# Kernel tuning notes

Measured on AMD Instinct MI355X. Metric: run time of the kernel, lower is better.

Reference implementation:

```python
import jax, jax.numpy as jnp
import numpy as np

N, M, D = 8192, 8192, 512

def setup_inputs() -> dict:
    key = jax.random.key(0)
    ks = jax.random.split(key, 8)
    s = 1.0 / np.sqrt(D)
    return {
        "x": jax.random.normal(ks[0], (N, D), jnp.float32),
        "domain_x": jax.random.normal(ks[1], (M, D), jnp.float32),
        "Wq": jax.random.normal(ks[2], (D, D), jnp.float32) * s,
        "bq": jax.random.normal(ks[3], (D,), jnp.float32) * s,
        "Wk": jax.random.normal(ks[4], (D, D), jnp.float32) * s,
        "bk": jax.random.normal(ks[5], (D,), jnp.float32) * s,
        "Wv": jax.random.normal(ks[6], (D, D), jnp.float32) * s,
        "bv": jax.random.normal(ks[7], (D,), jnp.float32) * s,
    }

def reference(x, domain_x, Wq, bq, Wk, bk, Wv, bv):
    # torch Linear: y = x @ W^T + b
    q = x @ Wq.T + bq            # [N, D]
    k = domain_x @ Wk.T + bk     # [M, D]
    v = domain_x @ Wv.T + bv     # [M, D]
    scale = jnp.sqrt(jnp.asarray(k.shape[-1], q.dtype))
    scores = q @ k.T             # [N, M]
    attn = jax.nn.softmax(scores / scale, axis=-1)
    return attn @ v              # [N, D]
```

## Files before the change

kernel.cpp:

```cpp
#include <hip/hip_runtime.h>
#include <stdint.h>


#define DEV __device__ __forceinline__

typedef short short8 __attribute__((ext_vector_type(8)));
typedef float floatx4 __attribute__((ext_vector_type(4)));
typedef unsigned int uintx4 __attribute__((ext_vector_type(4)));
typedef unsigned short ushortx4 __attribute__((ext_vector_type(4)));

constexpr int NN = 8192;
constexpr int MM = 8192;
constexpr int DD = 512;
constexpr float SCALE2 = 0.0637587160f;
constexpr float DEFER_THR = 6.0f;

#define NEG_INF (-__builtin_inff())

#if defined(__has_builtin)
#if __has_builtin(__builtin_amdgcn_exp2f)
#define EXP2F(x) __builtin_amdgcn_exp2f(x)
#else
#define EXP2F(x) exp2f(x)
#endif
#else
#define EXP2F(x) exp2f(x)
#endif

DEV unsigned short f2bf(float f) {
  unsigned u = __builtin_bit_cast(unsigned, f);
  return (unsigned short)((u + 0x7FFFu + ((u >> 16) & 1u)) >> 16);
}
DEV float bf2f(unsigned short h) {
  unsigned u = ((unsigned)h) << 16;
  return __builtin_bit_cast(float, u);
}

DEV short8 ld_s8(const void* p) {
  short8 v; __builtin_memcpy(&v, __builtin_assume_aligned(p, 16), 16); return v;
}
DEV uintx4 ld_u4(const void* p) {
  uintx4 v; __builtin_memcpy(&v, __builtin_assume_aligned(p, 16), 16); return v;
}
DEV void st_u4(void* p, uintx4 v) {
  __builtin_memcpy(__builtin_assume_aligned(p, 16), &v, 16);
}
DEV void st_us4(void* p, ushortx4 v) {
  __builtin_memcpy(__builtin_assume_aligned(p, 8), &v, 8);
}
DEV float4 ld_f4(const void* p) {
  float4 v; __builtin_memcpy(&v, __builtin_assume_aligned(p, 16), 16); return v;
}

DEV void async_lds16(const void* g, const void* l) {
  __builtin_amdgcn_global_load_lds(
      (const __attribute__((address_space(1))) unsigned int*)g,
      (__attribute__((address_space(3))) unsigned int*)l, 16, 0, 0);
}

__global__ void prep_w(const float* __restrict__ Wq, const float* __restrict__ Wk,
                       const float* __restrict__ Wv, unsigned short* __restrict__ Wb) {
  const int z = blockIdx.z;
  const float* src = (z == 0) ? Wq : (z == 1) ? Wk : Wv;
  unsigned short* dst = Wb + (size_t)z * DD * DD;
  size_t idx = ((size_t)blockIdx.x * 256 + threadIdx.x) * 8;
  float4 a = ld_f4(src + idx);
  float4 b = ld_f4(src + idx + 4);
  ushortx4 lo = {f2bf(a.x), f2bf(a.y), f2bf(a.z), f2bf(a.w)};
  ushortx4 hi = {f2bf(b.x), f2bf(b.y), f2bf(b.z), f2bf(b.w)};
  st_us4(dst + idx, lo);
  st_us4(dst + idx + 4, hi);
}

__global__ __launch_bounds__(256, 2)
void qkv_proj(const float* __restrict__ x, const float* __restrict__ dx,
              const unsigned short* __restrict__ Wb,
              const float* __restrict__ bq, const float* __restrict__ bk,
              const float* __restrict__ bv,
              unsigned short* __restrict__ Qb, unsigned short* __restrict__ Kb,
              unsigned short* __restrict__ VTb) {
  const int z = blockIdx.z;
  const float* A = (z == 0) ? x : dx;
  const unsigned short* W = Wb + (size_t)z * DD * DD;
  const float* bias = (z == 0) ? bq : (z == 1) ? bk : bv;

  const int r0 = blockIdx.x * 64;
  const int c0 = blockIdx.y * 256;
  const int tid = threadIdx.x;
  const int lane = tid & 63;
  const int wave = tid >> 6;
  const int lr = lane & 15;
  const int quad = lane >> 4;

  __shared__ __align__(16) unsigned short As[64 * 64];
  __shared__ __align__(16) unsigned short Ws[256 * 64];

  floatx4 o[16];
#pragma unroll
  for (int i = 0; i < 16; ++i) o[i] = {0.f, 0.f, 0.f, 0.f};

  for (int k0 = 0; k0 < DD; k0 += 64) {
#pragma unroll
    for (int i = 0; i < 4; ++i) {
      int idx = i * 256 + tid;
      int r = idx >> 4, c4 = idx & 15;
      float4 v = ld_f4(A + (size_t)(r0 + r) * DD + k0 + c4 * 4);
      ushortx4 pk = {f2bf(v.x), f2bf(v.y), f2bf(v.z), f2bf(v.w)};
      st_us4(&As[r * 64 + (((c4 >> 1) ^ (r & 7)) * 8) + (c4 & 1) * 4], pk);
    }
#pragma unroll
    for (int i = 0; i < 8; ++i) {
      int idx = i * 256 + tid;
      int r = idx >> 3, c = idx & 7;
      uintx4 v = ld_u4(W + (size_t)(c0 + r) * DD + k0 + c * 8);
      st_u4(&Ws[r * 64 + ((c ^ (r & 7)) * 8)], v);
    }
    __syncthreads();

    short8 a[2];
#pragma unroll
    for (int ks = 0; ks < 2; ++ks)
      a[ks] = ld_s8(&As[(wave * 16 + lr) * 64 + (((ks * 4 + quad) ^ (lr & 7)) * 8)]);
#pragma unroll
    for (int ct = 0; ct < 16; ++ct) {
#pragma unroll
      for (int ks = 0; ks < 2; ++ks) {
        short8 b = ld_s8(&Ws[(ct * 16 + lr) * 64 + (((ks * 4 + quad) ^ (lr & 7)) * 8)]);
        o[ct] = __builtin_amdgcn_mfma_f32_16x16x32_bf16(a[ks], b, o[ct], 0, 0, 0);
      }
    }
    __syncthreads();
  }

#pragma unroll
  for (int ct = 0; ct < 16; ++ct) {
    int col = c0 + ct * 16 + lr;
    float bv_ = bias[col];
    int rowb = r0 + wave * 16 + quad * 4;
    if (z == 2) {
      ushortx4 pk = {f2bf(o[ct][0] + bv_), f2bf(o[ct][1] + bv_),
                     f2bf(o[ct][2] + bv_), f2bf(o[ct][3] + bv_)};
      st_us4(VTb + (size_t)col * MM + rowb, pk);
    } else {
      unsigned short* Outp = (z == 0) ? Qb : Kb;
      float sc = (z == 0) ? SCALE2 : 1.f;
#pragma unroll
      for (int r = 0; r < 4; ++r)
        Outp[(size_t)(rowb + r) * DD + col] = f2bf((o[ct][r] + bv_) * sc);
    }
  }
}

template <int SPLITS_, int LOG2S_>
__global__ __launch_bounds__(256, 2)
void flash_attn(const unsigned short* __restrict__ Qb,
                const unsigned short* __restrict__ Kb,
                const unsigned short* __restrict__ VTb,
                unsigned short* __restrict__ Opart,
                float* __restrict__ Mpart, float* __restrict__ Lpart) {
  constexpr int MT = MM / SPLITS_;
  constexpr int ITERS = MT / 64;
  const int lin = blockIdx.x;
  const int split = lin & (SPLITS_ - 1);
  const int n0 = (lin >> LOG2S_) * 64;
  const int m_begin = split * MT;

  const int tid = threadIdx.x;
  const int lane = tid & 63;
  const int wave = tid >> 6;
  const int lr = lane & 15;
  const int quad = lane >> 4;

  __shared__ __align__(16) unsigned short sKV[33280];
  __shared__ __align__(16) unsigned short sP[64 * 76];
  __shared__ float sAlpha[64];
  __shared__ int sNeed;

  if (tid == 0) sNeed = 0;

  short8 qf[16];
  {
    const unsigned short* qptr = Qb + (size_t)(n0 + wave * 16 + lr) * DD + quad * 8;
#pragma unroll
    for (int ks = 0; ks < 16; ++ks) qf[ks] = ld_s8(qptr + ks * 32);
  }

  const int vrb = lane >> 3;
  const int vcb = ((lane & 7) ^ vrb) * 8;
  const unsigned short* vsrc0 = VTb + (size_t)(wave * 128 + vrb) * MM + vcb;
  unsigned short* vdst0 = &sKV[wave * 16 * 512];

  floatx4 o[32];
#pragma unroll
  for (int i = 0; i < 32; ++i) o[i] = {0.f, 0.f, 0.f, 0.f};
  float mrow[4] = {NEG_INF, NEG_INF, NEG_INF, NEG_INF};
  float lrow[4] = {0.f, 0.f, 0.f, 0.f};

  for (int it = 0; it < ITERS; ++it) {
    const int m0 = m_begin + it * 64;

#pragma unroll
    for (int i = 0; i < 16; ++i) {
      const int r = wave * 16 + i;
      async_lds16(Kb + (size_t)(m0 + r) * DD + lane * 8, &sKV[r * 520]);
    }
    __syncthreads();

    floatx4 s[4];
#pragma unroll
    for (int ct = 0; ct < 4; ++ct) s[ct] = {0.f, 0.f, 0.f, 0.f};
    __builtin_amdgcn_s_setprio(1);
#pragma unroll
    for (int ks = 0; ks < 16; ++ks) {
      const unsigned short* kb = &sKV[ks * 32 + quad * 8];
#pragma unroll
      for (int ct = 0; ct < 4; ++ct) {
        short8 b = ld_s8(kb + (ct * 16 + lr) * 520);
        s[ct] = __builtin_amdgcn_mfma_f32_16x16x32_bf16(qf[ks], b, s[ct], 0, 0, 0);
      }
    }
    __builtin_amdgcn_s_setprio(0);
    __syncthreads();

    {
      const unsigned short* src = vsrc0 + m0;
#pragma unroll
      for (int j = 0; j < 16; ++j)
        async_lds16(src + (size_t)j * 8 * MM, vdst0 + j * 512);
    }

    float alpha[4];
    bool anyresc = false;
#pragma unroll
    for (int r = 0; r < 4; ++r) {
      float mx = fmaxf(fmaxf(s[0][r], s[1][r]), fmaxf(s[2][r], s[3][r]));
      mx = fmaxf(mx, __shfl_xor(mx, 1));
      mx = fmaxf(mx, __shfl_xor(mx, 2));
      mx = fmaxf(mx, __shfl_xor(mx, 4));
      mx = fmaxf(mx, __shfl_xor(mx, 8));
      float mnew = (mx > mrow[r] + DEFER_THR) ? mx : mrow[r];
      alpha[r] = EXP2F(mrow[r] - mnew);
      anyresc = anyresc || (mnew != mrow[r]);
      mrow[r] = mnew;
      float rs = 0.f;
#pragma unroll
      for (int ct = 0; ct < 4; ++ct) {
        float p = EXP2F(s[ct][r] - mnew);
        s[ct][r] = p;
        rs += p;
      }
      rs += __shfl_xor(rs, 1);
      rs += __shfl_xor(rs, 2);
      rs += __shfl_xor(rs, 4);
      rs += __shfl_xor(rs, 8);
      lrow[r] = lrow[r] * alpha[r] + rs;
    }
    if (__any(anyresc)) {
      if (lane == 0) sNeed = 1;
    }
    if (lr == 0) {
#pragma unroll
      for (int r = 0; r < 4; ++r) sAlpha[wave * 16 + quad * 4 + r] = alpha[r];
    }

#pragma unroll
    for (int ct = 0; ct < 4; ++ct)
#pragma unroll
      for (int r = 0; r < 4; ++r)
        sP[(wave * 16 + quad * 4 + r) * 76 + ct * 16 + lr] = f2bf(s[ct][r]);

    __syncthreads();

    if (sNeed) {
      floatx4 af[4];
#pragma unroll
      for (int rt = 0; rt < 4; ++rt) {
        float4 t = ld_f4(&sAlpha[rt * 16 + quad * 4]);
        af[rt] = {t.x, t.y, t.z, t.w};
      }
#pragma unroll
      for (int rt = 0; rt < 4; ++rt)
#pragma unroll
        for (int ct = 0; ct < 8; ++ct)
#pragma unroll
          for (int r = 0; r < 4; ++r) o[rt * 8 + ct][r] *= af[rt][r];
    }

    __builtin_amdgcn_s_setprio(1);
#pragma unroll
    for (int ks = 0; ks < 2; ++ks) {
      short8 pa[4];
#pragma unroll
      for (int rt = 0; rt < 4; ++rt)
        pa[rt] = ld_s8(&sP[(rt * 16 + lr) * 76 + ks * 32 + quad * 8]);
#pragma unroll
      for (int ct = 0; ct < 8; ++ct) {
        const int r = wave * 128 + ct * 16 + lr;
        short8 b = ld_s8(&sKV[r * 64 + (((ks * 4 + quad) ^ (lr & 7)) * 8)]);
#pragma unroll
        for (int rt = 0; rt < 4; ++rt)
          o[rt * 8 + ct] = __builtin_amdgcn_mfma_f32_16x16x32_bf16(pa[rt], b,
                                                                   o[rt * 8 + ct], 0, 0, 0);
      }
    }
    __builtin_amdgcn_s_setprio(0);
    __syncthreads();
    if (tid == 0) sNeed = 0;
  }

  unsigned short* op = Opart + (size_t)split * NN * DD;
#pragma unroll
  for (int rt = 0; rt < 4; ++rt)
#pragma unroll
    for (int ct = 0; ct < 8; ++ct) {
      int row = n0 + rt * 16 + quad * 4;
      int col = wave * 128 + ct * 16 + lr;
#pragma unroll
      for (int r = 0; r < 4; ++r)
        op[(size_t)(row + r) * DD + col] = f2bf(o[rt * 8 + ct][r]);
    }
  const int grow = n0 + wave * 16 + quad * 4;
  if (lr == 0) {
#pragma unroll
    for (int r = 0; r < 4; ++r) {
      Mpart[split * NN + grow + r] = mrow[r];
      Lpart[split * NN + grow + r] = lrow[r];
    }
  }
}

template <int SPLITS_>
__global__ void combine_kernel(const unsigned short* __restrict__ Op,
                               const float* __restrict__ Mp,
                               const float* __restrict__ Lp,
                               float* __restrict__ out) {
  constexpr size_t NDv = (size_t)NN * DD;
  size_t base = ((size_t)blockIdx.x * 256 + threadIdx.x) * 8;
  int n = (int)(base >> 9);
  float mv[SPLITS_];
  float ms = NEG_INF;
#pragma unroll
  for (int s = 0; s < SPLITS_; ++s) {
    mv[s] = Mp[s * NN + n];
    ms = fmaxf(ms, mv[s]);
  }
  float num[8];
#pragma unroll
  for (int j = 0; j < 8; ++j) num[j] = 0.f;
  float den = 0.f;
#pragma unroll
  for (int s = 0; s < SPLITS_; ++s) {
    float w = EXP2F(mv[s] - ms);
    den += w * Lp[s * NN + n];
    uintx4 u = ld_u4(Op + s * NDv + base);
#pragma unroll
    for (int j = 0; j < 4; ++j) {
      num[2 * j]     += w * bf2f((unsigned short)(u[j] & 0xffffu));
      num[2 * j + 1] += w * bf2f((unsigned short)(u[j] >> 16));
    }
  }
  float inv = 1.f / den;
  float4 o0 = {num[0] * inv, num[1] * inv, num[2] * inv, num[3] * inv};
  float4 o1 = {num[4] * inv, num[5] * inv, num[6] * inv, num[7] * inv};
  __builtin_memcpy(__builtin_assume_aligned(out + base, 16), &o0, 16);
  __builtin_memcpy(__builtin_assume_aligned(out + base + 4, 16), &o1, 16);
}

extern "C" void kernel_launch(void* const* d_in, const int* in_sizes, int n_in,
                              void* d_out, int out_size, void* d_ws, size_t ws_size,
                              hipStream_t stream) {
  const float* x  = (const float*)d_in[0];
  const float* dx = (const float*)d_in[1];
  const float* Wq = (const float*)d_in[2];
  const float* bq = (const float*)d_in[3];
  const float* Wk = (const float*)d_in[4];
  const float* bk = (const float*)d_in[5];
  const float* Wv = (const float*)d_in[6];
  const float* bv = (const float*)d_in[7];
  float* out = (float*)d_out;

  const size_t ND = (size_t)NN * DD;
  const size_t WBE = (size_t)3 * DD * DD;
  unsigned short* Qb  = (unsigned short*)d_ws;
  unsigned short* Kb  = Qb + ND;
  unsigned short* VTb = Kb + ND;
  unsigned short* Wb  = VTb + ND;
  unsigned short* Op  = Wb + WBE;

  auto bytes_for = [&](size_t S) {
    return (3 * ND + WBE + S * ND) * 2 + S * (size_t)NN * 8;
  };
  const int splits = (ws_size >= bytes_for(4)) ? 4 : 2;
  float* Mp = (float*)(Op + (size_t)splits * ND);
  float* Lp = Mp + (size_t)splits * NN;

  hipLaunchKernelGGL(prep_w, dim3(DD * DD / 2048, 1, 3), dim3(256), 0, stream,
                     Wq, Wk, Wv, Wb);
  hipLaunchKernelGGL(qkv_proj, dim3(NN / 64, 2, 3), dim3(256), 0, stream,
                     x, dx, Wb, bq, bk, bv, Qb, Kb, VTb);
  if (splits == 4) {
    hipLaunchKernelGGL((flash_attn<4, 2>), dim3(NN / 64 * 4), dim3(256), 0, stream,
                       Qb, Kb, VTb, Op, Mp, Lp);
    hipLaunchKernelGGL(combine_kernel<4>, dim3((unsigned)(ND / 2048)), dim3(256), 0, stream,
                       Op, Mp, Lp, out);
  } else {
    hipLaunchKernelGGL((flash_attn<2, 1>), dim3(NN / 64 * 2), dim3(256), 0, stream,
                       Qb, Kb, VTb, Op, Mp, Lp);
    hipLaunchKernelGGL(combine_kernel<2>, dim3((unsigned)(ND / 2048)), dim3(256), 0, stream,
                       Op, Mp, Lp, out);
  }
}
```

Before: 337.4 us.

## Load V fragments directly from global in MFMA layout, prefetch next K tile

The V projection is now written in a blocked layout that matches the MFMA B-operand fragment order, so the PV product reads V straight from global memory into registers instead of staging it through LDS. The freed LDS buffer lets the next K tile be prefetched asynchronously during softmax, and the trailing barrier per iteration is removed by double-buffering the rescale flag. The sP row pitch drops from 76 to 72. This trades LDS traffic and barriers for more global/L2 loads on the critical path of the PV MFMAs, and may raise latency exposure or bank conflicts.

Measured after the change: 431.2 us. 27.8% more time.

```diff
diff --git a/kernel.cpp b/kernel.cpp
--- a/kernel.cpp
+++ b/kernel.cpp
@@ -14,6 +14,7 @@
 constexpr int DD = 512;
 constexpr float SCALE2 = 0.0637587160f;
 constexpr float DEFER_THR = 6.0f;
+constexpr int SP = 72;
 
 #define NEG_INF (-__builtin_inff())
 
@@ -140,7 +141,11 @@
     if (z == 2) {
       ushortx4 pk = {f2bf(o[ct][0] + bv_), f2bf(o[ct][1] + bv_),
                      f2bf(o[ct][2] + bv_), f2bf(o[ct][3] + bv_)};
-      st_us4(VTb + (size_t)col * MM + rowb, pk);
+      int dblk = col >> 4;
+      int mblk = rowb >> 5;
+      int lanep = ((rowb >> 3) & 3) * 16 + lr;
+      int e = rowb & 7;
+      st_us4(VTb + ((size_t)(dblk * 256 + mblk) * 64 + lanep) * 8 + e, pk);
     } else {
       unsigned short* Outp = (z == 0) ? Qb : Kb;
       float sc = (z == 0) ? SCALE2 : 1.f;
@@ -171,12 +176,12 @@
   const int lr = lane & 15;
   const int quad = lane >> 4;
 
-  __shared__ __align__(16) unsigned short sKV[33280];
-  __shared__ __align__(16) unsigned short sP[64 * 76];
+  __shared__ __align__(16) unsigned short sK[64 * 520];
+  __shared__ __align__(16) unsigned short sP[64 * SP];
   __shared__ float sAlpha[64];
-  __shared__ int sNeed;
-
-  if (tid == 0) sNeed = 0;
+  __shared__ int sNeed[2];
+
+  if (tid < 2) sNeed[tid] = 0;
 
   short8 qf[16];
   {
@@ -185,34 +190,29 @@
     for (int ks = 0; ks < 16; ++ks) qf[ks] = ld_s8(qptr + ks * 32);
   }
 
-  const int vrb = lane >> 3;
-  const int vcb = ((lane & 7) ^ vrb) * 8;
-  const unsigned short* vsrc0 = VTb + (size_t)(wave * 128 + vrb) * MM + vcb;
-  unsigned short* vdst0 = &sKV[wave * 16 * 512];
-
   floatx4 o[32];
 #pragma unroll
   for (int i = 0; i < 32; ++i) o[i] = {0.f, 0.f, 0.f, 0.f};
   float mrow[4] = {NEG_INF, NEG_INF, NEG_INF, NEG_INF};
   float lrow[4] = {0.f, 0.f, 0.f, 0.f};
 
+#pragma unroll
+  for (int i = 0; i < 16; ++i) {
+    const int r = wave * 16 + i;
+    async_lds16(Kb + (size_t)(m_begin + r) * DD + lane * 8, &sK[r * 520]);
+  }
+  __syncthreads();
+
   for (int it = 0; it < ITERS; ++it) {
     const int m0 = m_begin + it * 64;
 
-#pragma unroll
-    for (int i = 0; i < 16; ++i) {
-      const int r = wave * 16 + i;
-      async_lds16(Kb + (size_t)(m0 + r) * DD + lane * 8, &sKV[r * 520]);
-    }
-    __syncthreads();
-
     floatx4 s[4];
 #pragma unroll
     for (int ct = 0; ct < 4; ++ct) s[ct] = {0.f, 0.f, 0.f, 0.f};
     __builtin_amdgcn_s_setprio(1);
 #pragma unroll
     for (int ks = 0; ks < 16; ++ks) {
-      const unsigned short* kb = &sKV[ks * 32 + quad * 8];
+      const unsigned short* kb = &sK[ks * 32 + quad * 8];
 #pragma unroll
       for (int ct = 0; ct < 4; ++ct) {
         short8 b = ld_s8(kb + (ct * 16 + lr) * 520);
@@ -222,11 +222,12 @@
     __builtin_amdgcn_s_setprio(0);
     __syncthreads();
 
-    {
-      const unsigned short* src = vsrc0 + m0;
-#pragma unroll
-      for (int j = 0; j < 16; ++j)
-        async_lds16(src + (size_t)j * 8 * MM, vdst0 + j * 512);
+    if (it + 1 < ITERS) {
+#pragma unroll
+      for (int i = 0; i < 16; ++i) {
+        const int r = wave * 16 + i;
+        async_lds16(Kb + (size_t)(m0 + 64 + r) * DD + lane * 8, &sK[r * 520]);
+      }
     }
 
     float alpha[4];
@@ -256,8 +257,9 @@
       lrow[r] = lrow[r] * alpha[r] + rs;
     }
     if (__any(anyresc)) {
-      if (lane == 0) sNeed = 1;
-    }
+      if (lane == 0) sNeed[it & 1] = 1;
+    }
+    if (tid == 0) sNeed[(it + 1) & 1] = 0;
     if (lr == 0) {
 #pragma unroll
       for (int r = 0; r < 4; ++r) sAlpha[wave * 16 + quad * 4 + r] = alpha[r];
@@ -267,11 +269,11 @@
     for (int ct = 0; ct < 4; ++ct)
 #pragma unroll
       for (int r = 0; r < 4; ++r)
-        sP[(wave * 16 + quad * 4 + r) * 76 + ct * 16 + lr] = f2bf(s[ct][r]);
+        sP[(wave * 16 + quad * 4 + r) * SP + ct * 16 + lr] = f2bf(s[ct][r]);
 
     __syncthreads();
 
-    if (sNeed) {
+    if (sNeed[it & 1]) {
       floatx4 af[4];
 #pragma unroll
       for (int rt = 0; rt < 4; ++rt) {
@@ -286,17 +288,18 @@
           for (int r = 0; r < 4; ++r) o[rt * 8 + ct][r] *= af[rt][r];
     }
 
+    const unsigned short* vp =
+        VTb + (((size_t)wave * 8 * 256 + (m0 >> 5)) * 64 + lane) * 8;
     __builtin_amdgcn_s_setprio(1);
 #pragma unroll
     for (int ks = 0; ks < 2; ++ks) {
       short8 pa[4];
 #pragma unroll
       for (int rt = 0; rt < 4; ++rt)
-        pa[rt] = ld_s8(&sP[(rt * 16 + lr) * 76 + ks * 32 + quad * 8]);
+        pa[rt] = ld_s8(&sP[(rt * 16 + lr) * SP + ks * 32 + quad * 8]);
 #pragma unroll
       for (int ct = 0; ct < 8; ++ct) {
-        const int r = wave * 128 + ct * 16 + lr;
-        short8 b = ld_s8(&sKV[r * 64 + (((ks * 4 + quad) ^ (lr & 7)) * 8)]);
+        short8 b = ld_s8(vp + ((size_t)(ct * 256 + ks)) * 512);
 #pragma unroll
         for (int rt = 0; rt < 4; ++rt)
           o[rt * 8 + ct] = __builtin_amdgcn_mfma_f32_16x16x32_bf16(pa[rt], b,
@@ -304,8 +307,6 @@
       }
     }
     __builtin_amdgcn_s_setprio(0);
-    __syncthreads();
-    if (tid == 0) sNeed = 0;
   }
 
   unsigned short* op = Opart + (size_t)split * NN * DD;
```
